# Optimization experiments

Hardware: AMD Instinct MI355X
Metric: run time of the kernel (lower is better)

Reference implementation:

```python
import jax, jax.numpy as jnp
import numpy as np

# static config matching init_kwargs / input_specs
D = 768      # dim
H = 12       # num_heads
HD = D // H  # head_dim = 64
C = 38       # in_chans (AlternatingAttention default)
B = 4
T = 256
N = C * T    # 9728
SCALE = HD ** -0.5
EPS = 1e-5   # LayerNorm eps
HID = 4 * D  # mlp hidden


def setup_inputs() -> dict:
    key = jax.random.key(0)
    ks = jax.random.split(key, 6)
    w = lambda k, sh: (jax.random.normal(k, sh, jnp.float32) * 0.02)
    return {
        "x": jax.random.normal(ks[0], (B, N, D), jnp.float32),
        "norm1_w": jnp.ones((D,), jnp.float32),
        "norm1_b": jnp.zeros((D,), jnp.float32),
        "qkv_w": w(ks[1], (3 * D, D)),            # nn.Linear(dim, 3*dim, bias=False)
        "proj_w": w(ks[2], (D, D)),
        "proj_b": jnp.zeros((D,), jnp.float32),
        "norm2_w": jnp.ones((D,), jnp.float32),
        "norm2_b": jnp.zeros((D,), jnp.float32),
        "fc1_w": w(ks[3], (HID, D)),
        "fc1_b": jnp.zeros((HID,), jnp.float32),
        "fc2_w": w(ks[4], (D, HID)),
        "fc2_b": jnp.zeros((D,), jnp.float32),
    }


def _ln(x, w, b):
    m = x.mean(-1, keepdims=True)
    v = ((x - m) ** 2).mean(-1, keepdims=True)
    return (x - m) * jax.lax.rsqrt(v + EPS) * w + b


def _attn(x, qkv_w, proj_w, proj_b):
    # x: (Bc, Nn, D) -- manual (non-fused) SDPA as in the torch module
    Bc, Nn, _ = x.shape
    qkv = (x @ qkv_w.T).reshape(Bc, Nn, 3, H, HD)
    q, k, v = jnp.moveaxis(qkv, 2, 0)             # each (Bc, Nn, H, HD)
    q = jnp.swapaxes(q, 1, 2) * SCALE             # (Bc, H, Nn, HD)
    k = jnp.swapaxes(k, 1, 2)
    v = jnp.swapaxes(v, 1, 2)
    attn = jax.nn.softmax(q @ jnp.swapaxes(k, -2, -1), axis=-1)  # (Bc,H,Nn,Nn)
    o = attn @ v                                  # (Bc, H, Nn, HD)
    o = jnp.swapaxes(o, 1, 2).reshape(Bc, Nn, D)
    return o @ proj_w.T + proj_b


def reference(x, norm1_w, norm1_b, qkv_w, proj_w, proj_b,
              norm2_w, norm2_b, fc1_w, fc1_b, fc2_w, fc2_b):
    # Attention branch: block_idx=1 -> time-axis attention
    h = _ln(x, norm1_w, norm1_b)
    h = h.reshape(B, C, T, D).reshape(B * C, T, D)   # 'B (C T) D -> (B C) T D'
    h = _attn(h, qkv_w, proj_w, proj_b)
    h = h.reshape(B, C, T, D).reshape(B, N, D)       # '(B C) T D -> B (C T) D'
    x = x + h                                        # ls1 = Identity, drop_path = Identity
    # MLP branch
    h2 = _ln(x, norm2_w, norm2_b)
    h2 = jax.nn.gelu(h2 @ fc1_w.T + fc1_b, approximate=False)
    h2 = h2 @ fc2_w.T + fc2_b
    return x + h2
```

## Files before the change

### kernel.cpp

```cpp
#include <hip/hip_runtime.h>
#include <stdint.h>

#define DD 768
#define HH 12
#define HDIM 64
#define TT 256
#define BCN 152
#define MROWS 38912
#define HID 3072
#define MB_CNT 152

typedef __attribute__((ext_vector_type(8))) short bf16x8;
typedef __attribute__((ext_vector_type(4))) float f32x4;

__device__ __forceinline__ float b2f(unsigned short u) {
  union { unsigned int i; float f; } c; c.i = ((unsigned int)u) << 16; return c.f;
}
__device__ __forceinline__ unsigned short f2b(float f) {
  union { float f; unsigned int i; } c; c.f = f;
  unsigned int x = c.i;
  return (unsigned short)((x + 0x7fffu + ((x >> 16) & 1u)) >> 16);
}

__device__ __forceinline__ void gload16(const unsigned short* g, unsigned short* l) {
  __builtin_amdgcn_global_load_lds(
      (const __attribute__((address_space(1))) void*)g,
      (__attribute__((address_space(3))) void*)l, 16, 0, 0);
}

__global__ __launch_bounds__(256) void k_cvt(const float* __restrict__ in,
                                             unsigned short* __restrict__ out, int n4) {
  int i = blockIdx.x * 256 + threadIdx.x;
  if (i >= n4) return;
  float4 a = ((const float4*)in)[i];
  ushort4 u;
  u.x = f2b(a.x); u.y = f2b(a.y); u.z = f2b(a.z); u.w = f2b(a.w);
  ((ushort4*)out)[i] = u;
}

__global__ __launch_bounds__(256) void k_ln(const float* __restrict__ x,
                                            const float* __restrict__ w,
                                            const float* __restrict__ b,
                                            unsigned short* __restrict__ out) {
  int lane = threadIdx.x & 63;
  int wv = threadIdx.x >> 6;
  size_t row = (size_t)blockIdx.x * 4 + wv;
  const float4* xr = (const float4*)(x + row * DD);
  float4 v0 = xr[lane], v1 = xr[lane + 64], v2 = xr[lane + 128];
  float s = v0.x + v0.y + v0.z + v0.w + v1.x + v1.y + v1.z + v1.w + v2.x + v2.y + v2.z + v2.w;
  float q = v0.x*v0.x + v0.y*v0.y + v0.z*v0.z + v0.w*v0.w
          + v1.x*v1.x + v1.y*v1.y + v1.z*v1.z + v1.w*v1.w
          + v2.x*v2.x + v2.y*v2.y + v2.z*v2.z + v2.w*v2.w;
#pragma unroll
  for (int m = 1; m < 64; m <<= 1) { s += __shfl_xor(s, m, 64); q += __shfl_xor(q, m, 64); }
  float mean = s * (1.0f / 768.0f);
  float var = q * (1.0f / 768.0f) - mean * mean;
  float rstd = rsqrtf(var + 1e-5f);
  ushort4* orow = (ushort4*)(out + row * DD);
#pragma unroll
  for (int i = 0; i < 3; i++) {
    int idx = lane + i * 64;
    float4 v = (i == 0) ? v0 : (i == 1) ? v1 : v2;
    float4 ww = ((const float4*)w)[idx];
    float4 bb = ((const float4*)b)[idx];
    ushort4 u;
    u.x = f2b((v.x - mean) * rstd * ww.x + bb.x);
    u.y = f2b((v.y - mean) * rstd * ww.y + bb.y);
    u.z = f2b((v.z - mean) * rstd * ww.z + bb.z);
    u.w = f2b((v.w - mean) * rstd * ww.w + bb.w);
    orow[idx] = u;
  }
}


template <int MH>
__device__ __forceinline__ void read_a(const unsigned short* Al, bf16x8 (&af)[4][2],
                                       int wr, int cl, int hi) {
#pragma unroll
  for (int mi = 0; mi < 4; mi++)
#pragma unroll
    for (int ks = 0; ks < 2; ks++) {
      int row = MH * 128 + wr * 64 + mi * 16 + cl;
      af[mi][ks] = *(const bf16x8*)&Al[row * 64 + (((ks * 4 + hi) ^ (row & 7)) * 8)];
    }
}

template <int G>
__device__ __forceinline__ void read_b(const unsigned short* Bl, bf16x8 (&bfr)[2][2][2],
                                       int wc, int cl, int hi) {
#pragma unroll
  for (int ni = 0; ni < 2; ni++)
#pragma unroll
    for (int ks = 0; ks < 2; ks++) {
      int row = G * 128 + wc * 32 + ni * 16 + cl;
      bfr[G][ni][ks] = *(const bf16x8*)&Bl[row * 64 + (((ks * 4 + hi) ^ (row & 7)) * 8)];
    }
}

template <int MH, int G>
__device__ __forceinline__ void mfma_q(f32x4 (&acc)[2][4][2][2], const bf16x8 (&af)[4][2],
                                       const bf16x8 (&bfr)[2][2][2]) {
  __builtin_amdgcn_s_setprio(1);
#pragma unroll
  for (int mi = 0; mi < 4; mi++)
#pragma unroll
    for (int ni = 0; ni < 2; ni++)
#pragma unroll
      for (int ks = 0; ks < 2; ks++)
        acc[MH][mi][G][ni] = __builtin_amdgcn_mfma_f32_16x16x32_bf16(
            af[mi][ks], bfr[G][ni][ks], acc[MH][mi][G][ni], 0, 0, 0);
  __builtin_amdgcn_s_setprio(0);
}

#define VM4   asm volatile("s_waitcnt vmcnt(4)" ::: "memory")
#define LGKM0 do { asm volatile("s_waitcnt lgkmcnt(0)" ::: "memory"); \
                   __builtin_amdgcn_sched_barrier(0); } while (0)
#define BAR   __builtin_amdgcn_s_barrier()

template <int MODE>
__global__ __launch_bounds__(512, 1) void k_gemm4(const unsigned short* __restrict__ A,
                                                  const unsigned short* __restrict__ W,
                                                  const float* __restrict__ bias,
                                                  const float* resid,
                                                  void* outv, int N, int K, int NB) {
  __shared__ __align__(16) unsigned short As[2][256 * 64];
  __shared__ __align__(16) unsigned short Bs[2][256 * 64];
  const int tid = threadIdx.x;
  const int lane = tid & 63, wv = tid >> 6;
  const int wr = wv >> 2, wc = wv & 3;
  const int cl = lane & 15, hi = lane >> 4;

  const int b = blockIdx.x;
  const int bp = (b & 7) * 32 + (b >> 3);
  const int ntiles = MB_CNT * NB;
  const int q = ntiles >> 8, r = ntiles & 255;
  const int t0 = bp < r ? bp * (q + 1) : r * (q + 1) + (bp - r) * q;
  const int cnt = bp < r ? q + 1 : q;

  auto stA = [&](const unsigned short* base, int kt, int bb, int h) {
#pragma unroll
    for (int j = 0; j < 2; j++) {
      int idx = j * 512 + tid;
      int row = h * 128 + (idx >> 3);
      int cg = (idx & 7) ^ (row & 7);
      gload16(base + (size_t)row * K + (size_t)kt * 64 + cg * 8,
              &As[bb][row * 64 + (idx & 7) * 8]);
    }
  };
  auto stB = [&](const unsigned short* base, int kt, int bb, int h) {
#pragma unroll
    for (int j = 0; j < 2; j++) {
      int idx = j * 512 + tid;
      int row = h * 128 + (idx >> 3);
      int cg = (idx & 7) ^ (row & 7);
      gload16(base + (size_t)row * K + (size_t)kt * 64 + cg * 8,
              &Bs[bb][row * 64 + (idx & 7) * 8]);
    }
  };

  f32x4 acc[2][4][2][2];
  bf16x8 af[4][2], bfr[2][2][2];
  const int nt = K >> 6;

  for (int i = 0; i < cnt; i++) {
    const int tau = t0 + i;
    const int m_blk = tau % MB_CNT;
    const int n_blk = tau / MB_CNT;
    const size_t bm = (size_t)m_blk * 256, bn = (size_t)n_blk * 256;
    const unsigned short* Ab = A + bm * K;
    const unsigned short* Wb = W + bn * K;
    const bool hasNext = (i + 1 < cnt);
    const int tau2 = hasNext ? tau + 1 : tau;
    const unsigned short* An = A + (size_t)(tau2 % MB_CNT) * 256 * K;
    const unsigned short* Wn = W + (size_t)(tau2 / MB_CNT) * 256 * K;

#pragma unroll
    for (int a0 = 0; a0 < 2; a0++)
#pragma unroll
      for (int a1 = 0; a1 < 4; a1++)
#pragma unroll
        for (int a2 = 0; a2 < 2; a2++)
#pragma unroll
          for (int a3 = 0; a3 < 2; a3++) acc[a0][a1][a2][a3] = (f32x4){0.f, 0.f, 0.f, 0.f};

    if (i == 0) {
      stA(Ab, 0, 0, 0); stB(Wb, 0, 0, 0); stB(Wb, 0, 0, 1); stA(Ab, 0, 0, 1);
    }

    for (int t = 0; t < nt; t += 2) {
      const bool lastp = (t + 2 == nt);
      VM4; BAR;
      read_a<0>(As[0], af, wr, cl, hi);
      read_b<0>(Bs[0], bfr, wc, cl, hi);
      stA(Ab, t + 1, 1, 0);
      LGKM0;
      mfma_q<0, 0>(acc, af, bfr);
      VM4; BAR;
      read_b<1>(Bs[0], bfr, wc, cl, hi);
      stB(Wb, t + 1, 1, 0);
      LGKM0;
      mfma_q<0, 1>(acc, af, bfr);
      VM4; BAR;
      read_a<1>(As[0], af, wr, cl, hi);
      stB(Wb, t + 1, 1, 1);
      LGKM0;
      mfma_q<1, 0>(acc, af, bfr);
      BAR;
      stA(Ab, t + 1, 1, 1);
      mfma_q<1, 1>(acc, af, bfr);

      const bool st2 = !lastp || hasNext;
      const unsigned short* A2 = lastp ? An : Ab;
      const unsigned short* W2 = lastp ? Wn : Wb;
      const int k2 = lastp ? 0 : t + 2;
      VM4; BAR;
      read_a<0>(As[1], af, wr, cl, hi);
      read_b<0>(Bs[1], bfr, wc, cl, hi);
      if (st2) stA(A2, k2, 0, 0);
      LGKM0;
      mfma_q<0, 0>(acc, af, bfr);
      if (st2) { VM4; } else { asm volatile("s_waitcnt vmcnt(2)" ::: "memory"); }
      BAR;
      read_b<1>(Bs[1], bfr, wc, cl, hi);
      if (st2) stB(W2, k2, 0, 0);
      LGKM0;
      mfma_q<0, 1>(acc, af, bfr);
      if (st2) { VM4; } else { asm volatile("s_waitcnt vmcnt(0)" ::: "memory"); }
      BAR;
      read_a<1>(As[1], af, wr, cl, hi);
      if (st2) stB(W2, k2, 0, 1);
      LGKM0;
      mfma_q<1, 0>(acc, af, bfr);
      BAR;
      if (st2) stA(A2, k2, 0, 1);
      mfma_q<1, 1>(acc, af, bfr);
    }

#pragma unroll
    for (int mh = 0; mh < 2; mh++)
#pragma unroll
      for (int mi = 0; mi < 4; mi++)
#pragma unroll
        for (int g = 0; g < 2; g++)
#pragma unroll
          for (int ni = 0; ni < 2; ni++) {
            size_t col = bn + g * 128 + wc * 32 + ni * 16 + cl;
#pragma unroll
            for (int rr = 0; rr < 4; rr++) {
              size_t row = bm + mh * 128 + wr * 64 + mi * 16 + hi * 4 + rr;
              float v = acc[mh][mi][g][ni][rr];
              if (MODE == 0) {
                ((unsigned short*)outv)[row * N + col] = f2b(v);
              } else if (MODE == 1) {
                v += bias[col] + resid[row * N + col];
                ((float*)outv)[row * N + col] = v;
              } else {
                v += bias[col];
                float gg = 0.5f * v * (1.0f + erff(v * 0.70710678118654752f));
                ((unsigned short*)outv)[row * N + col] = f2b(gg);
              }
            }
          }
  }
}

__global__ __launch_bounds__(256) void k_attn(const unsigned short* __restrict__ qkv,
                                              unsigned short* __restrict__ o) {
  __shared__ unsigned short Kc[64 * 64];
  __shared__ unsigned short Vt[64 * 64];
  __shared__ unsigned short Pl[4][64 * 64];
  int h = blockIdx.x;
  int bc = blockIdx.y;
  int tid = threadIdx.x;
  int lane = tid & 63, wv = tid >> 6;
  int cl = lane & 15, hi = lane >> 4;

  bf16x8 qf[4][2];
#pragma unroll
  for (int m = 0; m < 4; m++)
#pragma unroll
    for (int ks = 0; ks < 2; ks++) {
      size_t row = (size_t)bc * 256 + wv * 64 + m * 16 + cl;
      bf16x8 raw = *(const bf16x8*)(qkv + row * 2304 + h * 64 + ks * 32 + hi * 8);
      bf16x8 sc;
#pragma unroll
      for (int j = 0; j < 8; j++) sc[j] = (short)f2b(0.125f * b2f((unsigned short)raw[j]));
      qf[m][ks] = sc;
    }

  f32x4 oacc[4][4];
#pragma unroll
  for (int m = 0; m < 4; m++)
#pragma unroll
    for (int n = 0; n < 4; n++) oacc[m][n] = (f32x4){0.f, 0.f, 0.f, 0.f};
  float mrun[4][4], lrun[4][4];
#pragma unroll
  for (int m = 0; m < 4; m++)
#pragma unroll
    for (int r = 0; r < 4; r++) { mrun[m][r] = -1e30f; lrun[m][r] = 0.f; }

  for (int j = 0; j < 4; j++) {
    __syncthreads();
#pragma unroll
    for (int it = 0; it < 2; ++it) {
      int idx = it * 256 + tid;
      int tok = idx >> 3;
      int c8 = idx & 7;
      size_t gtok = (size_t)bc * 256 + j * 64 + tok;
      uint4 kvv = *(const uint4*)(qkv + gtok * 2304 + 768 + h * 64 + c8 * 8);
      *(uint4*)&Kc[tok * 64 + c8 * 8] = kvv;
      union { uint4 u4; unsigned short us[8]; } cv;
      cv.u4 = *(const uint4*)(qkv + gtok * 2304 + 1536 + h * 64 + c8 * 8);
#pragma unroll
      for (int jj = 0; jj < 8; jj++) Vt[(c8 * 8 + jj) * 64 + tok] = cv.us[jj];
    }
    __syncthreads();

    f32x4 s[4][4];
#pragma unroll
    for (int m = 0; m < 4; m++)
#pragma unroll
      for (int n = 0; n < 4; n++) s[m][n] = (f32x4){0.f, 0.f, 0.f, 0.f};
#pragma unroll
    for (int ks = 0; ks < 2; ++ks) {
      int ko = ks * 32 + hi * 8;
      bf16x8 kf[4];
#pragma unroll
      for (int n = 0; n < 4; n++) kf[n] = *(const bf16x8*)&Kc[(n * 16 + cl) * 64 + ko];
#pragma unroll
      for (int m = 0; m < 4; m++)
#pragma unroll
        for (int n = 0; n < 4; n++)
          s[m][n] = __builtin_amdgcn_mfma_f32_16x16x32_bf16(qf[m][ks], kf[n], s[m][n], 0, 0, 0);
    }

#pragma unroll
    for (int m = 0; m < 4; m++) {
#pragma unroll
      for (int r = 0; r < 4; r++) {
        float pm = fmaxf(fmaxf(s[m][0][r], s[m][1][r]), fmaxf(s[m][2][r], s[m][3][r]));
#pragma unroll
        for (int xm = 1; xm < 16; xm <<= 1) pm = fmaxf(pm, __shfl_xor(pm, xm, 64));
        float nm = fmaxf(mrun[m][r], pm);
        float fac = __expf(mrun[m][r] - nm);
        mrun[m][r] = nm;
        float ps = 0.f;
#pragma unroll
        for (int n = 0; n < 4; n++) {
          float e = __expf(s[m][n][r] - nm);
          s[m][n][r] = e;
          ps += e;
        }
#pragma unroll
        for (int xm = 1; xm < 16; xm <<= 1) ps += __shfl_xor(ps, xm, 64);
        lrun[m][r] = lrun[m][r] * fac + ps;
#pragma unroll
        for (int n2 = 0; n2 < 4; n2++) oacc[m][n2][r] *= fac;
      }
#pragma unroll
      for (int n = 0; n < 4; n++)
#pragma unroll
        for (int r = 0; r < 4; r++)
          Pl[wv][(m * 16 + hi * 4 + r) * 64 + n * 16 + cl] = f2b(s[m][n][r]);
    }
    __syncthreads();

#pragma unroll
    for (int ks = 0; ks < 2; ++ks) {
      int ko = ks * 32 + hi * 8;
      bf16x8 pa[4], pv[4];
#pragma unroll
      for (int m = 0; m < 4; m++) pa[m] = *(const bf16x8*)&Pl[wv][(m * 16 + cl) * 64 + ko];
#pragma unroll
      for (int n = 0; n < 4; n++) pv[n] = *(const bf16x8*)&Vt[(n * 16 + cl) * 64 + ko];
#pragma unroll
      for (int m = 0; m < 4; m++)
#pragma unroll
        for (int n = 0; n < 4; n++)
          oacc[m][n] = __builtin_amdgcn_mfma_f32_16x16x32_bf16(pa[m], pv[n], oacc[m][n], 0, 0, 0);
    }
  }

#pragma unroll
  for (int m = 0; m < 4; m++)
#pragma unroll
    for (int r = 0; r < 4; r++) {
      float inv = 1.0f / lrun[m][r];
      size_t row = (size_t)bc * 256 + wv * 64 + m * 16 + hi * 4 + r;
#pragma unroll
      for (int n = 0; n < 4; n++)
        o[row * DD + h * 64 + n * 16 + cl] = f2b(oacc[m][n][r] * inv);
    }
}

extern "C" void kernel_launch(void* const* d_in, const int* in_sizes, int n_in,
                              void* d_out, int out_size, void* d_ws, size_t ws_size,
                              hipStream_t stream) {
  const float* x     = (const float*)d_in[0];
  const float* n1w   = (const float*)d_in[1];
  const float* n1b   = (const float*)d_in[2];
  const float* qkvw  = (const float*)d_in[3];
  const float* projw = (const float*)d_in[4];
  const float* projb = (const float*)d_in[5];
  const float* n2w   = (const float*)d_in[6];
  const float* n2b   = (const float*)d_in[7];
  const float* fc1w  = (const float*)d_in[8];
  const float* fc1b  = (const float*)d_in[9];
  const float* fc2w  = (const float*)d_in[10];
  const float* fc2b  = (const float*)d_in[11];
  float* out = (float*)d_out;

  const size_t NEED = 312999936ull;
  if (ws_size < NEED) return;
  char* ws = (char*)d_ws;
  unsigned short* h   = (unsigned short*)(ws);
  unsigned short* qkv = (unsigned short*)(ws + 59768832ull);
  unsigned short* ob  = (unsigned short*)(ws + 239075328ull);
  unsigned short* act = (unsigned short*)(ws + 59768832ull);
  unsigned short* wq  = (unsigned short*)(ws + 298844160ull);
  unsigned short* wp  = wq + 2304 * 768;
  unsigned short* w1  = wp + 768 * 768;
  unsigned short* w2  = w1 + 3072 * 768;

  k_cvt<<<1728, 256, 0, stream>>>(qkvw, wq, 2304 * 768 / 4);
  k_cvt<<<576, 256, 0, stream>>>(projw, wp, 768 * 768 / 4);
  k_cvt<<<2304, 256, 0, stream>>>(fc1w, w1, 3072 * 768 / 4);
  k_cvt<<<2304, 256, 0, stream>>>(fc2w, w2, 768 * 3072 / 4);

  k_ln<<<MROWS / 4, 256, 0, stream>>>(x, n1w, n1b, h);
  k_gemm4<0><<<256, 512, 0, stream>>>(h, wq, nullptr, nullptr, qkv, 2304, 768, 9);
  k_attn<<<dim3(HH, BCN), 256, 0, stream>>>(qkv, ob);
  k_gemm4<1><<<256, 512, 0, stream>>>(ob, wp, projb, x, out, 768, 768, 3);
  k_ln<<<MROWS / 4, 256, 0, stream>>>(out, n2w, n2b, h);
  k_gemm4<2><<<256, 512, 0, stream>>>(h, w1, fc1b, nullptr, act, 3072, 768, 12);
  k_gemm4<1><<<256, 512, 0, stream>>>(act, w2, fc2b, out, out, 768, 3072, 3);
}
```

Baseline: 1.221 ms.

## Deepen GEMM global-load prefetch and switch tile order to N-fastest

Reworks the persistent GEMM's load schedule so global loads for the next K step are issued further ahead (prologue preloads two K tiles, waits use vmcnt(6) and fewer waits per half-step). Tile traversal changes from M-fastest to N-fastest, so consecutive tiles processed by a block share the A row panel. The aim is to hide more global memory latency behind MFMA work and improve L2 reuse. The cost is more loads in flight and a more delicate LDS buffer-reuse ordering, which could introduce races if the barrier placement no longer protects the overwritten halves.

```diff
diff --git a/kernel.cpp b/kernel.cpp
--- a/kernel.cpp
+++ b/kernel.cpp
@@ -112,13 +112,14 @@
   __builtin_amdgcn_s_setprio(0);
 }
 
-#define VM4   asm volatile("s_waitcnt vmcnt(4)" ::: "memory")
+#define VM6   asm volatile("s_waitcnt vmcnt(6)" ::: "memory")
+#define VM0   asm volatile("s_waitcnt vmcnt(0)" ::: "memory")
 #define LGKM0 do { asm volatile("s_waitcnt lgkmcnt(0)" ::: "memory"); \
                    __builtin_amdgcn_sched_barrier(0); } while (0)
 #define BAR   __builtin_amdgcn_s_barrier()
 
 template <int MODE>
-__global__ __launch_bounds__(512, 1) void k_gemm4(const unsigned short* __restrict__ A,
+__global__ __launch_bounds__(512, 1) void k_gemm5(const unsigned short* __restrict__ A,
                                                   const unsigned short* __restrict__ W,
                                                   const float* __restrict__ bias,
                                                   const float* resid,
@@ -164,15 +165,15 @@
 
   for (int i = 0; i < cnt; i++) {
     const int tau = t0 + i;
-    const int m_blk = tau % MB_CNT;
-    const int n_blk = tau / MB_CNT;
+    const int m_blk = tau / NB;
+    const int n_blk = tau % NB;
     const size_t bm = (size_t)m_blk * 256, bn = (size_t)n_blk * 256;
     const unsigned short* Ab = A + bm * K;
     const unsigned short* Wb = W + bn * K;
     const bool hasNext = (i + 1 < cnt);
     const int tau2 = hasNext ? tau + 1 : tau;
-    const unsigned short* An = A + (size_t)(tau2 % MB_CNT) * 256 * K;
-    const unsigned short* Wn = W + (size_t)(tau2 / MB_CNT) * 256 * K;
+    const unsigned short* An = A + (size_t)(tau2 / NB) * 256 * K;
+    const unsigned short* Wn = W + (size_t)(tau2 % NB) * 256 * K;
 
 #pragma unroll
     for (int a0 = 0; a0 < 2; a0++)
@@ -185,54 +186,56 @@
 
     if (i == 0) {
       stA(Ab, 0, 0, 0); stB(Wb, 0, 0, 0); stB(Wb, 0, 0, 1); stA(Ab, 0, 0, 1);
+      stA(Ab, 1, 1, 0); stB(Wb, 1, 1, 0); stB(Wb, 1, 1, 1);
     }
 
     for (int t = 0; t < nt; t += 2) {
-      const bool lastp = (t + 2 == nt);
-      VM4; BAR;
+      const bool seam = (t + 2 == nt);
+      const bool last = seam && !hasNext;
+      const unsigned short* A2 = seam ? An : Ab;
+      const unsigned short* W2 = seam ? Wn : Wb;
+      const int k2 = seam ? 0 : t + 2;
+      const int k3 = seam ? 1 : t + 3;
+
+      VM6; BAR;
       read_a<0>(As[0], af, wr, cl, hi);
       read_b<0>(Bs[0], bfr, wc, cl, hi);
-      stA(Ab, t + 1, 1, 0);
+      stA(Ab, t + 1, 1, 1);
       LGKM0;
       mfma_q<0, 0>(acc, af, bfr);
-      VM4; BAR;
+      BAR;
       read_b<1>(Bs[0], bfr, wc, cl, hi);
-      stB(Wb, t + 1, 1, 0);
+      if (!last) stA(A2, k2, 0, 0);
       LGKM0;
       mfma_q<0, 1>(acc, af, bfr);
-      VM4; BAR;
+      BAR;
       read_a<1>(As[0], af, wr, cl, hi);
-      stB(Wb, t + 1, 1, 1);
+      if (!last) stB(W2, k2, 0, 0);
       LGKM0;
       mfma_q<1, 0>(acc, af, bfr);
       BAR;
-      stA(Ab, t + 1, 1, 1);
+      if (!last) stB(W2, k2, 0, 1);
       mfma_q<1, 1>(acc, af, bfr);
 
-      const bool st2 = !lastp || hasNext;
-      const unsigned short* A2 = lastp ? An : Ab;
-      const unsigned short* W2 = lastp ? Wn : Wb;
-      const int k2 = lastp ? 0 : t + 2;
-      VM4; BAR;
+      if (last) { VM0; } else { VM6; }
+      BAR;
       read_a<0>(As[1], af, wr, cl, hi);
       read_b<0>(Bs[1], bfr, wc, cl, hi);
-      if (st2) stA(A2, k2, 0, 0);
+      if (!last) stA(A2, k2, 0, 1);
       LGKM0;
       mfma_q<0, 0>(acc, af, bfr);
-      if (st2) { VM4; } else { asm volatile("s_waitcnt vmcnt(2)" ::: "memory"); }
       BAR;
       read_b<1>(Bs[1], bfr, wc, cl, hi);
-      if (st2) stB(W2, k2, 0, 0);
+      if (!last) stA(A2, k3, 1, 0);
       LGKM0;
       mfma_q<0, 1>(acc, af, bfr);
-      if (st2) { VM4; } else { asm volatile("s_waitcnt vmcnt(0)" ::: "memory"); }
       BAR;
       read_a<1>(As[1], af, wr, cl, hi);
-      if (st2) stB(W2, k2, 0, 1);
+      if (!last) stB(W2, k3, 1, 0);
       LGKM0;
       mfma_q<1, 0>(acc, af, bfr);
       BAR;
-      if (st2) stA(A2, k2, 0, 1);
+      if (!last) stB(W2, k3, 1, 1);
       mfma_q<1, 1>(acc, af, bfr);
     }
 
@@ -428,10 +431,10 @@
   k_cvt<<<2304, 256, 0, stream>>>(fc2w, w2, 768 * 3072 / 4);
 
   k_ln<<<MROWS / 4, 256, 0, stream>>>(x, n1w, n1b, h);
-  k_gemm4<0><<<256, 512, 0, stream>>>(h, wq, nullptr, nullptr, qkv, 2304, 768, 9);
+  k_gemm5<0><<<256, 512, 0, stream>>>(h, wq, nullptr, nullptr, qkv, 2304, 768, 9);
   k_attn<<<dim3(HH, BCN), 256, 0, stream>>>(qkv, ob);
-  k_gemm4<1><<<256, 512, 0, stream>>>(ob, wp, projb, x, out, 768, 768, 3);
+  k_gemm5<1><<<256, 512, 0, stream>>>(ob, wp, projb, x, out, 768, 768, 3);
   k_ln<<<MROWS / 4, 256, 0, stream>>>(out, n2w, n2b, h);
-  k_gemm4<2><<<256, 512, 0, stream>>>(h, w1, fc1b, nullptr, act, 3072, 768, 12);
-  k_gemm4<1><<<256, 512, 0, stream>>>(act, w2, fc2b, out, out, 768, 3072, 3);
-}
+  k_gemm5<2><<<256, 512, 0, stream>>>(h, w1, fc1b, nullptr, act, 3072, 768, 12);
+  k_gemm5<1><<<256, 512, 0, stream>>>(act, w2, fc2b, out, out, 768, 3072, 3);
+}
```

New measurement: 1.243 ms. No clear change (+1.8%).
